# Performance work log

Hardware: AMD Instinct MI355X
Metric: run time of the kernel (lower is better)

The kernel has to match this reference:

```python
import jax, jax.numpy as jnp
import numpy as np

B, N, F_IN, D, NBLOCKS = 16, 1024, 3, 128, 15
EPS = 1e-5


def setup_inputs() -> dict:
    key = jax.random.key(0)
    ks = jax.random.split(key, 8)
    inputs = jax.random.normal(ks[0], (B, N, F_IN), dtype=jnp.float32)
    # Row-normalized random adjacency as the graph operator L (spectral norm <= 1)
    A = jax.random.uniform(ks[1], (B, N, N), dtype=jnp.float32)
    L = A / jnp.sum(A, axis=-1, keepdims=True)
    mask = (jax.random.uniform(ks[2], (B, N, 1)) < 0.8).astype(jnp.float32)
    mask = mask.at[:, 0, :].set(1.0)  # ensure no empty graph
    W1 = jax.random.normal(ks[3], (F_IN, D), dtype=jnp.float32) / np.sqrt(F_IN)
    b1 = jnp.zeros((D,), jnp.float32)
    W_blocks = jax.random.normal(ks[4], (NBLOCKS, D, D), dtype=jnp.float32) / np.sqrt(D)
    b_blocks = jnp.zeros((NBLOCKS, D), jnp.float32)
    gamma_blocks = jnp.ones((NBLOCKS, D), jnp.float32)
    beta_blocks = jnp.zeros((NBLOCKS, D), jnp.float32)
    gamma1 = jnp.ones((D,), jnp.float32)
    beta1 = jnp.zeros((D,), jnp.float32)
    gamma2 = jnp.ones((D,), jnp.float32)
    beta2 = jnp.zeros((D,), jnp.float32)
    W2 = jax.random.normal(ks[5], (D, D), dtype=jnp.float32) / np.sqrt(D)
    b2 = jnp.zeros((D,), jnp.float32)
    return dict(inputs=inputs, L=L, mask=mask, W1=W1, b1=b1,
                W_blocks=W_blocks, b_blocks=b_blocks,
                gamma_blocks=gamma_blocks, beta_blocks=beta_blocks,
                gamma1=gamma1, beta1=beta1, gamma2=gamma2, beta2=beta2,
                W2=W2, b2=b2)


def _graph_bn(x, gamma, beta):
    # BatchNorm over (batch, nodes) per feature channel (training-mode stats)
    mean = jnp.mean(x, axis=(0, 1), keepdims=True)
    var = jnp.var(x, axis=(0, 1), keepdims=True)
    return (x - mean) * jax.lax.rsqrt(var + EPS) * gamma + beta


def reference(inputs, L, mask, W1, b1, W_blocks, b_blocks,
              gamma_blocks, beta_blocks, gamma1, beta1, gamma2, beta2,
              W2, b2):
    # conv1 (GraphConv k=1): per-node linear
    x1 = jnp.einsum('bnf,fd->bnd', inputs, W1) + b1          # [B,N,D]
    x2 = jnp.zeros_like(x1)

    def step(carry, params):
        a, b_prev = carry
        W, bias, g, be = params
        h = jax.nn.elu(_graph_bn(a, g, be))
        h = jnp.einsum('bnm,bmd->bnd', L, h)                 # Laplacian aggregation
        h = jnp.einsum('bnd,de->bne', h, W) + bias           # LapConv transform
        return (b_prev + h, a), None

    (x1, x2), _ = jax.lax.scan(step, (x1, x2),
                               (W_blocks, b_blocks, gamma_blocks, beta_blocks))

    x = jax.nn.elu(_graph_bn(x1, gamma1, beta1) + _graph_bn(x2, gamma2, beta2))
    # Dropout2d is identity in deterministic/eval reference
    x = jnp.einsum('bnd,de->bne', x, W2) + b2                # conv2 (k=1)
    # masked mean pool over nodes: mask [B,N,1] broadcasts over D
    out = jnp.sum(x * mask, axis=1) / jnp.sum(mask, axis=1)  # [B,D]
    return out
```

## Files before the change

### kernel.cpp

```cpp
#include <hip/hip_runtime.h>

typedef float f32x4 __attribute__((ext_vector_type(4)));
typedef __bf16 bf16x8 __attribute__((ext_vector_type(8)));
typedef unsigned int u32x4 __attribute__((ext_vector_type(4)));
typedef unsigned int u32x2 __attribute__((ext_vector_type(2)));
typedef unsigned short u16;

#define DEV __device__ __forceinline__

DEV u16 f2bf(float f) {
    unsigned int x = __float_as_uint(f);
    x += 0x7fffu + ((x >> 16) & 1u);
    return (u16)(x >> 16);
}
DEV unsigned pk2(float a, float b) {
    return (unsigned)f2bf(a) | ((unsigned)f2bf(b) << 16);
}
DEV float elu(float x) { return x > 0.f ? x : expm1f(x); }

DEV void gload16(const u16* g, void* l) {
    __builtin_amdgcn_global_load_lds(
        (const __attribute__((address_space(1))) unsigned int*)g,
        (__attribute__((address_space(3))) unsigned int*)l,
        16, 0, 0);
}

constexpr float INV_M = 1.f / 16384.f;
constexpr float EPSV  = 1e-5f;


__global__ void k_cvt_bf16(const float* __restrict__ src, u16* __restrict__ dst) {
    long i = ((long)blockIdx.x * 256 + threadIdx.x) * 8;
    f32x4 a = *(const f32x4*)(src + i);
    f32x4 b = *(const f32x4*)(src + i + 4);
    u32x4 v;
    v[0] = pk2(a[0], a[1]); v[1] = pk2(a[2], a[3]);
    v[2] = pk2(b[0], b[1]); v[3] = pk2(b[2], b[3]);
    *(u32x4*)(dst + i) = v;
}

__global__ void k_cvt_wt(const float* __restrict__ W, u16* __restrict__ WT,
                         float* __restrict__ SP0, float* __restrict__ SP1) {
    int o = blockIdx.x * 256 + threadIdx.x;
    int k = o >> 14, r = o & 16383, e = r >> 7, d = r & 127;
    WT[o] = f2bf(W[(k << 14) + (d << 7) + e]);
    if (blockIdx.x < 32) {
        float* z = blockIdx.x < 16 ? SP0 : SP1;
        z[(blockIdx.x & 15) * 256 + threadIdx.x] = 0.f;
    }
}

__global__ __launch_bounds__(256) void k_init(
        const float* __restrict__ in, const float* __restrict__ W1,
        const float* __restrict__ b1, float* __restrict__ x1,
        float* __restrict__ x2, float* __restrict__ sp) {
    __shared__ float red[2][8][128];
    int t = threadIdx.x;
    long R = (long)blockIdx.x * 64;
    int c4 = (t & 31) * 4, rg = t >> 5;
    float w0[4], w1[4], w2[4], bb4[4];
#pragma unroll
    for (int c = 0; c < 4; ++c) {
        w0[c] = W1[c4 + c]; w1[c] = W1[128 + c4 + c]; w2[c] = W1[256 + c4 + c];
        bb4[c] = b1[c4 + c];
    }
    float s[4] = {}, q[4] = {};
    for (int i = 0; i < 8; ++i) {
        long grow = R + rg + 8 * i;
        float f0 = in[grow * 3], f1 = in[grow * 3 + 1], f2 = in[grow * 3 + 2];
        f32x4 v, z = {0.f, 0.f, 0.f, 0.f};
#pragma unroll
        for (int c = 0; c < 4; ++c) {
            float val = f0 * w0[c] + f1 * w1[c] + f2 * w2[c] + bb4[c];
            v[c] = val; s[c] += val; q[c] += val * val;
        }
        *(f32x4*)(x1 + grow * 128 + c4) = v;
        *(f32x4*)(x2 + grow * 128 + c4) = z;
    }
#pragma unroll
    for (int c = 0; c < 4; ++c) { red[0][rg][c4 + c] = s[c]; red[1][rg][c4 + c] = q[c]; }
    __syncthreads();
    if (t < 128) {
        float a = 0;
#pragma unroll
        for (int g = 0; g < 8; ++g) a += red[0][g][t];
        atomicAdd(&sp[(blockIdx.x & 15) * 256 + t], a);
    } else {
        int c = t - 128; float a = 0;
#pragma unroll
        for (int g = 0; g < 8; ++g) a += red[1][g][c];
        atomicAdd(&sp[(blockIdx.x & 15) * 256 + 128 + c], a);
    }
}


__global__ __launch_bounds__(256) void k_bnelu(
        const float* __restrict__ x, const float* __restrict__ spa,
        float* __restrict__ spb_zero,
        const float* __restrict__ gamma, const float* __restrict__ beta,
        const u16* __restrict__ WTk, u16* __restrict__ hT) {
    __shared__ u16 Hs[8192];
    __shared__ u16 Ws[16384];
    __shared__ float st[256];
    __shared__ float sc[128], sh[128];
    int t = threadIdx.x;
    int R = blockIdx.x * 64;  int bb = R >> 10, n0 = R & 1023;
    int l = t & 63, w = t >> 6;
    int wm = w >> 1, wn = w & 1;
    int l16 = l & 15, ld16 = l >> 4;

    {
        float s = 0.f;
#pragma unroll
        for (int i = 0; i < 16; ++i) s += spa[i * 256 + t];
        st[t] = s;
    }
    if (blockIdx.x < 16) spb_zero[blockIdx.x * 256 + t] = 0.f;

    {
        const u32x4* wsrc = (const u32x4*)WTk;
#pragma unroll
        for (int i = 0; i < 8; ++i) {
            int u = t + 256 * i;
            int r = u >> 4, sl = u & 15;
            *(u32x4*)((char*)Ws + r * 256 + ((sl ^ (r & 7)) << 4)) = wsrc[u];
        }
    }
    __syncthreads();
    if (t < 128) {
        float mean = st[t] * INV_M, var = st[128 + t] * INV_M - mean * mean;
        float a = rsqrtf(var + EPSV) * gamma[t];
        sc[t] = a; sh[t] = beta[t] - mean * a;
    }
    __syncthreads();

    {
        const float* xb = x + (long)R * 128;
#pragma unroll
        for (int i = 0; i < 8; ++i) {
            int idx = t + 256 * i;
            int row = idx >> 5, c4 = (idx & 31) * 4;
            f32x4 v = *(const f32x4*)(xb + row * 128 + c4);
            float h0 = elu(v[0] * sc[c4]     + sh[c4]);
            float h1 = elu(v[1] * sc[c4 + 1] + sh[c4 + 1]);
            float h2 = elu(v[2] * sc[c4 + 2] + sh[c4 + 2]);
            float h3 = elu(v[3] * sc[c4 + 3] + sh[c4 + 3]);
            u32x2 pw = {pk2(h0, h1), pk2(h2, h3)};
            *(u32x2*)((char*)Hs + row * 256 + ((c4 * 2) ^ ((row & 7) << 4))) = pw;
        }
    }
    __syncthreads();

    f32x4 acc[2][4] = {};
#pragma unroll
    for (int ks = 0; ks < 4; ++ks) {
        int kb = ks * 64 + ld16 * 16;
        bf16x8 af[2], bfr[4];
#pragma unroll
        for (int m = 0; m < 2; ++m) {
            int r = wm * 32 + m * 16 + l16;
            af[m] = *(const bf16x8*)((char*)Hs + r * 256 + (kb ^ ((r & 7) << 4)));
        }
#pragma unroll
        for (int n = 0; n < 4; ++n) {
            int e = wn * 64 + n * 16 + l16;
            bfr[n] = *(const bf16x8*)((char*)Ws + e * 256 + (kb ^ ((e & 7) << 4)));
        }
#pragma unroll
        for (int m = 0; m < 2; ++m)
#pragma unroll
            for (int n = 0; n < 4; ++n)
                acc[m][n] = __builtin_amdgcn_mfma_f32_16x16x32_bf16(
                    af[m], bfr[n], acc[m][n], 0, 0, 0);
    }
    __syncthreads();

#pragma unroll
    for (int m = 0; m < 2; ++m)
#pragma unroll
        for (int n = 0; n < 4; ++n) {
            int e = wn * 64 + n * 16 + l16;
            int row0 = wm * 32 + m * 16 + ld16 * 4;
            u32x2 pw = {pk2(acc[m][n][0], acc[m][n][1]),
                        pk2(acc[m][n][2], acc[m][n][3])};
            *(u32x2*)((char*)Hs + e * 128 + ((row0 * 2) ^ ((e & 7) << 4))) = pw;
        }
    __syncthreads();

    {
        int e = t >> 1, sg = t & 1;
        const char* base = (const char*)Hs + e * 128;
        u16* orow = hT + ((long)(bb * 128 + e)) * 1024 + n0 + sg * 32;
#pragma unroll
        for (int u = 0; u < 4; ++u) {
            u32x4 v = *(const u32x4*)(base + ((((sg * 4 + u) * 16)) ^ ((e & 7) << 4)));
            *(u32x4*)(orow + u * 8) = v;
        }
    }
}

__global__ __launch_bounds__(512) void k_gemm(
        const u16* __restrict__ Lb, const u16* __restrict__ hT,
        const float* __restrict__ bias, float* __restrict__ xio,
        float* __restrict__ spb) {
    __shared__ u16 As[3][4096];
    __shared__ u16 Bs[3][8192];
    __shared__ float red[2][8][128];

    int t = threadIdx.x;
    int bid0 = blockIdx.x;
    int wg = ((bid0 & 7) << 5) | (bid0 >> 3);
    int bb = wg >> 4, n0 = (wg & 15) << 6;
    int l = t & 63, w = t >> 6;
    int wm = w >> 2, wn = w & 3;
    int l16 = l & 15, ld16 = l >> 4;

    const u16* gA = Lb + ((long)(bb * 1024 + n0)) * 1024;
    const u16* gB = hT + (long)bb * 131072;

#define STAGE(buf, kt) do {                                                   \
        int k0_ = (kt) * 64;                                                  \
        { int u = t; int r = u >> 3, sl = u & 7;                              \
          gload16(gA + (long)r * 1024 + k0_ + ((sl ^ (r & 7)) << 3),          \
                  (char*)As[buf] + u * 16); }                                 \
        _Pragma("unroll")                                                     \
        for (int j = 0; j < 2; ++j) {                                         \
            int u = t + 512 * j; int r = u >> 3, sl = u & 7;                  \
            gload16(gB + (long)r * 1024 + k0_ + ((sl ^ (r & 7)) << 3),        \
                    (char*)Bs[buf] + u * 16);                                 \
        }                                                                     \
    } while (0)

    f32x4 acc[2][2] = {};

    STAGE(0, 0);
    STAGE(1, 1);
    asm volatile("s_waitcnt vmcnt(3)" ::: "memory");
    __builtin_amdgcn_s_barrier();

    for (int kt = 0; kt < 16; ++kt) {
        if (kt <= 13) STAGE((kt + 2) % 3, kt + 2);
        const char* Ab = (const char*)(As[kt % 3]);
        const char* Bb = (const char*)(Bs[kt % 3]);
        __builtin_amdgcn_s_setprio(1);
#pragma unroll
        for (int ks = 0; ks < 2; ++ks) {
            int kb = ks * 64 + ld16 * 16;
            bf16x8 af[2], bfr[2];
#pragma unroll
            for (int m = 0; m < 2; ++m) {
                int r = wm * 32 + m * 16 + l16;
                af[m] = *(const bf16x8*)(Ab + r * 128 + (kb ^ ((r & 7) << 4)));
            }
#pragma unroll
            for (int n = 0; n < 2; ++n) {
                int e = wn * 32 + n * 16 + l16;
                bfr[n] = *(const bf16x8*)(Bb + e * 128 + (kb ^ ((e & 7) << 4)));
            }
#pragma unroll
            for (int m = 0; m < 2; ++m)
#pragma unroll
                for (int n = 0; n < 2; ++n)
                    acc[m][n] = __builtin_amdgcn_mfma_f32_16x16x32_bf16(
                        af[m], bfr[n], acc[m][n], 0, 0, 0);
        }
        __builtin_amdgcn_s_setprio(0);
        if (kt <= 13) {
            asm volatile("s_waitcnt vmcnt(3)" ::: "memory");
            __builtin_amdgcn_s_barrier();
        } else if (kt == 14) {
            asm volatile("s_waitcnt vmcnt(0)" ::: "memory");
            __builtin_amdgcn_s_barrier();
        }
    }
#undef STAGE

    float* dst = xio + (long)(bb * 1024 + n0) * 128;
#pragma unroll
    for (int n = 0; n < 2; ++n) {
        int e = wn * 32 + n * 16 + l16;
        float bv = bias[e];
        float sv = 0.f, qv = 0.f;
#pragma unroll
        for (int m = 0; m < 2; ++m) {
            int row0 = wm * 32 + m * 16 + ld16 * 4;
            float* dp = dst + (long)row0 * 128 + e;
#pragma unroll
            for (int j = 0; j < 4; ++j) {
                float v = dp[j * 128] + acc[m][n][j] + bv;
                dp[j * 128] = v;
                sv += v; qv += v * v;
            }
        }
        red[0][wm * 4 + ld16][e] = sv;
        red[1][wm * 4 + ld16][e] = qv;
    }
    __syncthreads();
    if (t < 128) {
        float a = 0;
#pragma unroll
        for (int g = 0; g < 8; ++g) a += red[0][g][t];
        atomicAdd(&spb[(bid0 & 15) * 256 + t], a);
    } else if (t < 256) {
        int c = t - 128; float a = 0;
#pragma unroll
        for (int g = 0; g < 8; ++g) a += red[1][g][c];
        atomicAdd(&spb[(bid0 & 15) * 256 + 128 + c], a);
    }
}


__global__ void k_redstats2(const float* __restrict__ sp1, const float* __restrict__ sp0,
                            const float* __restrict__ g1, const float* __restrict__ be1,
                            const float* __restrict__ g2, const float* __restrict__ be2,
                            float* __restrict__ scb2) {
    int t = threadIdx.x;
    int which = t >> 7, c = t & 127;
    const float* p = which ? sp0 : sp1;
    float s = 0.f, q = 0.f;
#pragma unroll
    for (int i = 0; i < 16; ++i) { s += p[i * 256 + c]; q += p[i * 256 + 128 + c]; }
    float mean = s * INV_M, var = q * INV_M - mean * mean;
    const float* g = which ? g2 : g1; const float* be = which ? be2 : be1;
    float a = rsqrtf(var + EPSV) * g[c];
    scb2[which * 256 + c] = a;
    scb2[which * 256 + 128 + c] = be[c] - mean * a;
}

__global__ void k_finalpool(const float* __restrict__ x1, const float* __restrict__ x2,
                            const float* __restrict__ scb2, const float* __restrict__ mask,
                            float* __restrict__ poolP, float* __restrict__ maskP) {
    __shared__ float sc1[128], sh1[128], sc2[128], sh2[128];
    __shared__ float red[8][128];
    __shared__ float msk[64];
    int t = threadIdx.x;
    int R = blockIdx.x * 64, bb = R >> 10, tl = (R & 1023) >> 6;
    if (t < 128) {
        sc1[t] = scb2[t];       sh1[t] = scb2[128 + t];
        sc2[t] = scb2[256 + t]; sh2[t] = scb2[384 + t];
    }
    if (t >= 128 && t < 192) msk[t - 128] = mask[bb * 1024 + (R & 1023) + (t - 128)];
    __syncthreads();
    const float* xb1 = x1 + (long)R * 128;
    const float* xb2 = x2 + (long)R * 128;
    int row0 = t >> 5, c = (t & 31) * 4;
    f32x4 accv = {0.f, 0.f, 0.f, 0.f};
    for (int i = 0; i < 8; ++i) {
        int row = row0 + 8 * i;
        f32x4 v1 = *(const f32x4*)(xb1 + row * 128 + c);
        f32x4 v2 = *(const f32x4*)(xb2 + row * 128 + c);
        float m = msk[row];
        accv[0] += elu(v1[0]*sc1[c]   + sh1[c]   + v2[0]*sc2[c]   + sh2[c])   * m;
        accv[1] += elu(v1[1]*sc1[c+1] + sh1[c+1] + v2[1]*sc2[c+1] + sh2[c+1]) * m;
        accv[2] += elu(v1[2]*sc1[c+2] + sh1[c+2] + v2[2]*sc2[c+2] + sh2[c+2]) * m;
        accv[3] += elu(v1[3]*sc1[c+3] + sh1[c+3] + v2[3]*sc2[c+3] + sh2[c+3]) * m;
    }
    red[row0][c] = accv[0]; red[row0][c+1] = accv[1];
    red[row0][c+2] = accv[2]; red[row0][c+3] = accv[3];
    __syncthreads();
    if (t < 128) {
        float s = 0;
#pragma unroll
        for (int g = 0; g < 8; ++g) s += red[g][t];
        poolP[(bb * 16 + tl) * 128 + t] = s;
    }
    if (t == 0) {
        float sm = 0;
        for (int j = 0; j < 64; ++j) sm += msk[j];
        maskP[bb * 16 + tl] = sm;
    }
}

__global__ void k_out(const float* __restrict__ poolP, const float* __restrict__ maskP,
                      const float* __restrict__ W2, const float* __restrict__ b2,
                      float* __restrict__ out) {
    int bb = blockIdx.x, t = threadIdx.x;
    __shared__ float pooled[128];
    __shared__ float inv;
    float s = 0;
    for (int tl = 0; tl < 16; ++tl) s += poolP[(bb * 16 + tl) * 128 + t];
    pooled[t] = s;
    if (t == 0) {
        float sm = 0;
        for (int tl = 0; tl < 16; ++tl) sm += maskP[bb * 16 + tl];
        inv = 1.f / sm;
    }
    __syncthreads();
    float acc = 0;
    for (int d = 0; d < 128; ++d) acc += pooled[d] * W2[d * 128 + t];
    out[bb * 128 + t] = acc * inv + b2[t];
}


extern "C" void kernel_launch(void* const* d_in, const int* in_sizes, int n_in,
                              void* d_out, int out_size, void* d_ws, size_t ws_size,
                              hipStream_t stream) {
    const float* inputs = (const float*)d_in[0];
    const float* L      = (const float*)d_in[1];
    const float* mask   = (const float*)d_in[2];
    const float* W1     = (const float*)d_in[3];
    const float* b1     = (const float*)d_in[4];
    const float* Wb     = (const float*)d_in[5];
    const float* bblk   = (const float*)d_in[6];
    const float* gb     = (const float*)d_in[7];
    const float* beb    = (const float*)d_in[8];
    const float* g1     = (const float*)d_in[9];
    const float* be1    = (const float*)d_in[10];
    const float* g2     = (const float*)d_in[11];
    const float* be2    = (const float*)d_in[12];
    const float* W2     = (const float*)d_in[13];
    const float* b2     = (const float*)d_in[14];
    float* out = (float*)d_out;

    char* ws = (char*)d_ws;
    u16*   Lb    = (u16*)(ws);
    u16*   WT    = (u16*)(ws + 33554432);
    float* xA    = (float*)(ws + 34045952);
    float* xB    = (float*)(ws + 42434560);
    u16*   hT    = (u16*)(ws + 50823168);
    float* SP0   = (float*)(ws + 55017472);
    float* SP1   = (float*)(ws + 55279616);
    float* scb2  = (float*)(ws + 55542784);
    float* poolP = (float*)(ws + 50823168);
    float* maskP = (float*)(ws + 50823168 + 131072);
    float* SP[2] = {SP0, SP1};

    hipLaunchKernelGGL(k_cvt_bf16, dim3(8192), dim3(256), 0, stream, L, Lb);
    hipLaunchKernelGGL(k_cvt_wt,   dim3(960),  dim3(256), 0, stream, Wb, WT, SP0, SP1);
    hipLaunchKernelGGL(k_init,     dim3(256),  dim3(256), 0, stream,
                       inputs, W1, b1, xA, xB, SP0);

    float* pa = xA; float* pb = xB;
    for (int k = 0; k < 15; ++k) {
        hipLaunchKernelGGL(k_bnelu, dim3(256), dim3(256), 0, stream,
                           pa, SP[k & 1], SP[(k + 1) & 1],
                           gb + k * 128, beb + k * 128,
                           WT + (size_t)k * 16384, hT);
        hipLaunchKernelGGL(k_gemm, dim3(256), dim3(512), 0, stream,
                           Lb, hT, bblk + k * 128, pb, SP[(k + 1) & 1]);
        float* tmp = pa; pa = pb; pb = tmp;
    }
    hipLaunchKernelGGL(k_redstats2, dim3(1), dim3(256), 0, stream,
                       SP[1], SP[0], g1, be1, g2, be2, scb2);
    hipLaunchKernelGGL(k_finalpool, dim3(256), dim3(256), 0, stream,
                       pa, pb, scb2, mask, poolP, maskP);
    hipLaunchKernelGGL(k_out, dim3(16), dim3(128), 0, stream, poolP, maskP, W2, b2, out);
}
```

Before: 394.0 us.

## Fuse all stages into one persistent kernel with software grid barriers

Replaces the sequence of about 35 kernel launches (conversion, init, 15 pairs of bnelu and gemm, final stats, pool, output) with one persistent 256-block kernel that separates phases with an atomic-counter grid barrier. The goal is to remove launch overhead and the inter-kernel gaps between the many short stages. The bnelu stage now runs with 512 threads per block and a different warp tiling, and the final stats are computed redundantly per block. In exchange it relies on all 256 blocks being co-resident, and adds spin-wait barrier cost at every phase.

```diff
diff --git a/kernel.cpp b/kernel.cpp
--- a/kernel.cpp
+++ b/kernel.cpp
@@ -25,370 +25,372 @@
         16, 0, 0);
 }
 
+DEV void gridbar(unsigned* bar) {
+    __syncthreads();
+    if (threadIdx.x == 0) {
+        __builtin_amdgcn_fence(__ATOMIC_RELEASE, "agent");
+        unsigned old = __hip_atomic_fetch_add(bar, 1u, __ATOMIC_RELAXED,
+                                              __HIP_MEMORY_SCOPE_AGENT);
+        unsigned target = ((old >> 8) << 8) + 256u;
+        while (__hip_atomic_load(bar, __ATOMIC_RELAXED,
+                                 __HIP_MEMORY_SCOPE_AGENT) < target)
+            __builtin_amdgcn_s_sleep(2);
+        __builtin_amdgcn_fence(__ATOMIC_ACQUIRE, "agent");
+    }
+    __syncthreads();
+}
+
 constexpr float INV_M = 1.f / 16384.f;
 constexpr float EPSV  = 1e-5f;
 
-
-__global__ void k_cvt_bf16(const float* __restrict__ src, u16* __restrict__ dst) {
-    long i = ((long)blockIdx.x * 256 + threadIdx.x) * 8;
-    f32x4 a = *(const f32x4*)(src + i);
-    f32x4 b = *(const f32x4*)(src + i + 4);
-    u32x4 v;
-    v[0] = pk2(a[0], a[1]); v[1] = pk2(a[2], a[3]);
-    v[2] = pk2(b[0], b[1]); v[3] = pk2(b[2], b[3]);
-    *(u32x4*)(dst + i) = v;
-}
-
-__global__ void k_cvt_wt(const float* __restrict__ W, u16* __restrict__ WT,
-                         float* __restrict__ SP0, float* __restrict__ SP1) {
-    int o = blockIdx.x * 256 + threadIdx.x;
-    int k = o >> 14, r = o & 16383, e = r >> 7, d = r & 127;
-    WT[o] = f2bf(W[(k << 14) + (d << 7) + e]);
-    if (blockIdx.x < 32) {
-        float* z = blockIdx.x < 16 ? SP0 : SP1;
-        z[(blockIdx.x & 15) * 256 + threadIdx.x] = 0.f;
-    }
-}
-
-__global__ __launch_bounds__(256) void k_init(
-        const float* __restrict__ in, const float* __restrict__ W1,
-        const float* __restrict__ b1, float* __restrict__ x1,
-        float* __restrict__ x2, float* __restrict__ sp) {
-    __shared__ float red[2][8][128];
+__global__ __launch_bounds__(512) void k_mega(
+        const float* __restrict__ in, const float* __restrict__ L,
+        const float* __restrict__ mask, const float* __restrict__ W1,
+        const float* __restrict__ b1, const float* __restrict__ Wb,
+        const float* __restrict__ bblk, const float* __restrict__ gb,
+        const float* __restrict__ beb, const float* __restrict__ g1,
+        const float* __restrict__ be1, const float* __restrict__ g2,
+        const float* __restrict__ be2, const float* __restrict__ W2,
+        const float* __restrict__ b2,
+        u16* __restrict__ Lb, u16* __restrict__ WT,
+        float* __restrict__ xA, float* __restrict__ xB,
+        u16* __restrict__ hT, float* __restrict__ SP0, float* __restrict__ SP1,
+        unsigned* __restrict__ bar, float* __restrict__ poolP,
+        float* __restrict__ maskP, float* __restrict__ out) {
+    extern __shared__ char smem[];
     int t = threadIdx.x;
-    long R = (long)blockIdx.x * 64;
-    int c4 = (t & 31) * 4, rg = t >> 5;
-    float w0[4], w1[4], w2[4], bb4[4];
-#pragma unroll
-    for (int c = 0; c < 4; ++c) {
-        w0[c] = W1[c4 + c]; w1[c] = W1[128 + c4 + c]; w2[c] = W1[256 + c4 + c];
-        bb4[c] = b1[c4 + c];
-    }
-    float s[4] = {}, q[4] = {};
-    for (int i = 0; i < 8; ++i) {
-        long grow = R + rg + 8 * i;
-        float f0 = in[grow * 3], f1 = in[grow * 3 + 1], f2 = in[grow * 3 + 2];
-        f32x4 v, z = {0.f, 0.f, 0.f, 0.f};
-#pragma unroll
-        for (int c = 0; c < 4; ++c) {
-            float val = f0 * w0[c] + f1 * w1[c] + f2 * w2[c] + bb4[c];
-            v[c] = val; s[c] += val; q[c] += val * val;
-        }
-        *(f32x4*)(x1 + grow * 128 + c4) = v;
-        *(f32x4*)(x2 + grow * 128 + c4) = z;
-    }
-#pragma unroll
-    for (int c = 0; c < 4; ++c) { red[0][rg][c4 + c] = s[c]; red[1][rg][c4 + c] = q[c]; }
-    __syncthreads();
-    if (t < 128) {
-        float a = 0;
-#pragma unroll
-        for (int g = 0; g < 8; ++g) a += red[0][g][t];
-        atomicAdd(&sp[(blockIdx.x & 15) * 256 + t], a);
-    } else {
-        int c = t - 128; float a = 0;
-#pragma unroll
-        for (int g = 0; g < 8; ++g) a += red[1][g][c];
-        atomicAdd(&sp[(blockIdx.x & 15) * 256 + 128 + c], a);
-    }
-}
-
-
-__global__ __launch_bounds__(256) void k_bnelu(
-        const float* __restrict__ x, const float* __restrict__ spa,
-        float* __restrict__ spb_zero,
-        const float* __restrict__ gamma, const float* __restrict__ beta,
-        const u16* __restrict__ WTk, u16* __restrict__ hT) {
-    __shared__ u16 Hs[8192];
-    __shared__ u16 Ws[16384];
-    __shared__ float st[256];
-    __shared__ float sc[128], sh[128];
-    int t = threadIdx.x;
-    int R = blockIdx.x * 64;  int bb = R >> 10, n0 = R & 1023;
-    int l = t & 63, w = t >> 6;
-    int wm = w >> 1, wn = w & 1;
-    int l16 = l & 15, ld16 = l >> 4;
-
-    {
-        float s = 0.f;
-#pragma unroll
-        for (int i = 0; i < 16; ++i) s += spa[i * 256 + t];
-        st[t] = s;
-    }
-    if (blockIdx.x < 16) spb_zero[blockIdx.x * 256 + t] = 0.f;
-
-    {
-        const u32x4* wsrc = (const u32x4*)WTk;
-#pragma unroll
-        for (int i = 0; i < 8; ++i) {
-            int u = t + 256 * i;
-            int r = u >> 4, sl = u & 15;
-            *(u32x4*)((char*)Ws + r * 256 + ((sl ^ (r & 7)) << 4)) = wsrc[u];
-        }
-    }
-    __syncthreads();
-    if (t < 128) {
-        float mean = st[t] * INV_M, var = st[128 + t] * INV_M - mean * mean;
-        float a = rsqrtf(var + EPSV) * gamma[t];
-        sc[t] = a; sh[t] = beta[t] - mean * a;
-    }
-    __syncthreads();
-
-    {
-        const float* xb = x + (long)R * 128;
-#pragma unroll
-        for (int i = 0; i < 8; ++i) {
-            int idx = t + 256 * i;
-            int row = idx >> 5, c4 = (idx & 31) * 4;
-            f32x4 v = *(const f32x4*)(xb + row * 128 + c4);
-            float h0 = elu(v[0] * sc[c4]     + sh[c4]);
-            float h1 = elu(v[1] * sc[c4 + 1] + sh[c4 + 1]);
-            float h2 = elu(v[2] * sc[c4 + 2] + sh[c4 + 2]);
-            float h3 = elu(v[3] * sc[c4 + 3] + sh[c4 + 3]);
-            u32x2 pw = {pk2(h0, h1), pk2(h2, h3)};
-            *(u32x2*)((char*)Hs + row * 256 + ((c4 * 2) ^ ((row & 7) << 4))) = pw;
-        }
-    }
-    __syncthreads();
-
-    f32x4 acc[2][4] = {};
-#pragma unroll
-    for (int ks = 0; ks < 4; ++ks) {
-        int kb = ks * 64 + ld16 * 16;
-        bf16x8 af[2], bfr[4];
-#pragma unroll
-        for (int m = 0; m < 2; ++m) {
-            int r = wm * 32 + m * 16 + l16;
-            af[m] = *(const bf16x8*)((char*)Hs + r * 256 + (kb ^ ((r & 7) << 4)));
-        }
-#pragma unroll
-        for (int n = 0; n < 4; ++n) {
-            int e = wn * 64 + n * 16 + l16;
-            bfr[n] = *(const bf16x8*)((char*)Ws + e * 256 + (kb ^ ((e & 7) << 4)));
-        }
-#pragma unroll
-        for (int m = 0; m < 2; ++m)
-#pragma unroll
-            for (int n = 0; n < 4; ++n)
-                acc[m][n] = __builtin_amdgcn_mfma_f32_16x16x32_bf16(
-                    af[m], bfr[n], acc[m][n], 0, 0, 0);
-    }
-    __syncthreads();
-
-#pragma unroll
-    for (int m = 0; m < 2; ++m)
-#pragma unroll
-        for (int n = 0; n < 4; ++n) {
-            int e = wn * 64 + n * 16 + l16;
-            int row0 = wm * 32 + m * 16 + ld16 * 4;
-            u32x2 pw = {pk2(acc[m][n][0], acc[m][n][1]),
-                        pk2(acc[m][n][2], acc[m][n][3])};
-            *(u32x2*)((char*)Hs + e * 128 + ((row0 * 2) ^ ((e & 7) << 4))) = pw;
-        }
-    __syncthreads();
-
-    {
-        int e = t >> 1, sg = t & 1;
-        const char* base = (const char*)Hs + e * 128;
-        u16* orow = hT + ((long)(bb * 128 + e)) * 1024 + n0 + sg * 32;
-#pragma unroll
-        for (int u = 0; u < 4; ++u) {
-            u32x4 v = *(const u32x4*)(base + ((((sg * 4 + u) * 16)) ^ ((e & 7) << 4)));
-            *(u32x4*)(orow + u * 8) = v;
-        }
-    }
-}
-
-__global__ __launch_bounds__(512) void k_gemm(
-        const u16* __restrict__ Lb, const u16* __restrict__ hT,
-        const float* __restrict__ bias, float* __restrict__ xio,
-        float* __restrict__ spb) {
-    __shared__ u16 As[3][4096];
-    __shared__ u16 Bs[3][8192];
-    __shared__ float red[2][8][128];
-
-    int t = threadIdx.x;
-    int bid0 = blockIdx.x;
-    int wg = ((bid0 & 7) << 5) | (bid0 >> 3);
+    int bid = blockIdx.x;
+    int wg = ((bid & 7) << 5) | (bid >> 3);
     int bb = wg >> 4, n0 = (wg & 15) << 6;
     int l = t & 63, w = t >> 6;
     int wm = w >> 2, wn = w & 3;
     int l16 = l & 15, ld16 = l >> 4;
 
-    const u16* gA = Lb + ((long)(bb * 1024 + n0)) * 1024;
-    const u16* gB = hT + (long)bb * 131072;
-
-#define STAGE(buf, kt) do {                                                   \
-        int k0_ = (kt) * 64;                                                  \
-        { int u = t; int r = u >> 3, sl = u & 7;                              \
-          gload16(gA + (long)r * 1024 + k0_ + ((sl ^ (r & 7)) << 3),          \
-                  (char*)As[buf] + u * 16); }                                 \
-        _Pragma("unroll")                                                     \
-        for (int j = 0; j < 2; ++j) {                                         \
-            int u = t + 512 * j; int r = u >> 3, sl = u & 7;                  \
-            gload16(gB + (long)r * 1024 + k0_ + ((sl ^ (r & 7)) << 3),        \
-                    (char*)Bs[buf] + u * 16);                                 \
-        }                                                                     \
-    } while (0)
-
-    f32x4 acc[2][2] = {};
-
-    STAGE(0, 0);
-    STAGE(1, 1);
-    asm volatile("s_waitcnt vmcnt(3)" ::: "memory");
-    __builtin_amdgcn_s_barrier();
-
-    for (int kt = 0; kt < 16; ++kt) {
-        if (kt <= 13) STAGE((kt + 2) % 3, kt + 2);
-        const char* Ab = (const char*)(As[kt % 3]);
-        const char* Bb = (const char*)(Bs[kt % 3]);
-        __builtin_amdgcn_s_setprio(1);
-#pragma unroll
-        for (int ks = 0; ks < 2; ++ks) {
-            int kb = ks * 64 + ld16 * 16;
-            bf16x8 af[2], bfr[2];
-#pragma unroll
-            for (int m = 0; m < 2; ++m) {
-                int r = wm * 32 + m * 16 + l16;
-                af[m] = *(const bf16x8*)(Ab + r * 128 + (kb ^ ((r & 7) << 4)));
-            }
+    {
+        for (long v = (long)bid * 512 + t; v < 2097152; v += 131072) {
+            long i = v * 8;
+            f32x4 a = *(const f32x4*)(L + i);
+            f32x4 b = *(const f32x4*)(L + i + 4);
+            u32x4 pv;
+            pv[0] = pk2(a[0], a[1]); pv[1] = pk2(a[2], a[3]);
+            pv[2] = pk2(b[0], b[1]); pv[3] = pk2(b[2], b[3]);
+            *(u32x4*)(Lb + i) = pv;
+        }
+        for (int o = bid * 512 + t; o < 245760; o += 131072) {
+            int k = o >> 14, r = o & 16383, e = r >> 7, d = r & 127;
+            WT[o] = f2bf(Wb[(k << 14) + (d << 7) + e]);
+        }
+        float* red0 = (float*)smem;
+        float* red1 = (float*)(smem + 8192);
+        int c4 = (t & 31) * 4, rg = t >> 5;
+        float w0[4], w1v[4], w2v[4], bb4[4];
+#pragma unroll
+        for (int c = 0; c < 4; ++c) {
+            w0[c] = W1[c4 + c]; w1v[c] = W1[128 + c4 + c];
+            w2v[c] = W1[256 + c4 + c]; bb4[c] = b1[c4 + c];
+        }
+        float s[4] = {}, q[4] = {};
+        long R = (long)wg * 64;
+#pragma unroll
+        for (int i = 0; i < 4; ++i) {
+            long grow = R + rg + 16 * i;
+            float f0 = in[grow * 3], f1 = in[grow * 3 + 1], f2 = in[grow * 3 + 2];
+            f32x4 v, z = {0.f, 0.f, 0.f, 0.f};
+#pragma unroll
+            for (int c = 0; c < 4; ++c) {
+                float val = f0 * w0[c] + f1 * w1v[c] + f2 * w2v[c] + bb4[c];
+                v[c] = val; s[c] += val; q[c] += val * val;
+            }
+            *(f32x4*)(xA + grow * 128 + c4) = v;
+            *(f32x4*)(xB + grow * 128 + c4) = z;
+        }
+#pragma unroll
+        for (int c = 0; c < 4; ++c) {
+            red0[rg * 128 + c4 + c] = s[c]; red1[rg * 128 + c4 + c] = q[c];
+        }
+        __syncthreads();
+        if (t < 128) {
+            float a = 0;
+#pragma unroll
+            for (int g = 0; g < 16; ++g) a += red0[g * 128 + t];
+            atomicAdd(&SP0[(wg & 15) * 256 + t], a);
+        } else if (t < 256) {
+            int c = t - 128; float a = 0;
+#pragma unroll
+            for (int g = 0; g < 16; ++g) a += red1[g * 128 + c];
+            atomicAdd(&SP0[(wg & 15) * 256 + 128 + c], a);
+        }
+    }
+    gridbar(bar);
+
+    float* pa = xA; float* pb = xB;
+    for (int k = 0; k < 15; ++k) {
+        float* spa = (k & 1) ? SP1 : SP0;
+        float* spb = (k & 1) ? SP0 : SP1;
+
+        {
+            u16* Ws = (u16*)smem;
+            u16* Hs = (u16*)(smem + 32768);
+            float* st = (float*)(smem + 49152);
+            float* sc = (float*)(smem + 50176);
+            float* sh = (float*)(smem + 50688);
+            if (t < 256) {
+                float s = 0.f;
+#pragma unroll
+                for (int i = 0; i < 16; ++i) s += spa[i * 256 + t];
+                st[t] = s;
+            }
+            if (wg < 16 && t < 256) spb[wg * 256 + t] = 0.f;
+            const u32x4* wsrc = (const u32x4*)(WT + (size_t)k * 16384);
+#pragma unroll
+            for (int i = 0; i < 4; ++i) {
+                int u = t + 512 * i;
+                int r = u >> 4, sl = u & 15;
+                *(u32x4*)((char*)Ws + r * 256 + ((sl ^ (r & 7)) << 4)) = wsrc[u];
+            }
+            __syncthreads();
+            if (t < 128) {
+                float mean = st[t] * INV_M, var = st[128 + t] * INV_M - mean * mean;
+                float a = rsqrtf(var + EPSV) * gb[k * 128 + t];
+                sc[t] = a; sh[t] = beb[k * 128 + t] - mean * a;
+            }
+            __syncthreads();
+            const float* xb = pa + (long)wg * 8192;
+#pragma unroll
+            for (int i = 0; i < 4; ++i) {
+                int idx = t + 512 * i;
+                int row = idx >> 5, c4 = (idx & 31) * 4;
+                f32x4 v = *(const f32x4*)(xb + row * 128 + c4);
+                float h0 = elu(v[0] * sc[c4]     + sh[c4]);
+                float h1 = elu(v[1] * sc[c4 + 1] + sh[c4 + 1]);
+                float h2 = elu(v[2] * sc[c4 + 2] + sh[c4 + 2]);
+                float h3 = elu(v[3] * sc[c4 + 3] + sh[c4 + 3]);
+                u32x2 pw = {pk2(h0, h1), pk2(h2, h3)};
+                *(u32x2*)((char*)Hs + row * 256 + ((c4 * 2) ^ ((row & 7) << 4))) = pw;
+            }
+            __syncthreads();
+            f32x4 acc[2][2] = {};
+#pragma unroll
+            for (int ks = 0; ks < 4; ++ks) {
+                int kb = ks * 64 + ld16 * 16;
+                bf16x8 af[2], bfr[2];
+#pragma unroll
+                for (int m = 0; m < 2; ++m) {
+                    int r = wm * 32 + m * 16 + l16;
+                    af[m] = *(const bf16x8*)((char*)Hs + r * 256 + (kb ^ ((r & 7) << 4)));
+                }
+#pragma unroll
+                for (int n = 0; n < 2; ++n) {
+                    int e = wn * 32 + n * 16 + l16;
+                    bfr[n] = *(const bf16x8*)((char*)Ws + e * 256 + (kb ^ ((e & 7) << 4)));
+                }
+#pragma unroll
+                for (int m = 0; m < 2; ++m)
+#pragma unroll
+                    for (int n = 0; n < 2; ++n)
+                        acc[m][n] = __builtin_amdgcn_mfma_f32_16x16x32_bf16(
+                            af[m], bfr[n], acc[m][n], 0, 0, 0);
+            }
+            __syncthreads();
+#pragma unroll
+            for (int m = 0; m < 2; ++m)
+#pragma unroll
+                for (int n = 0; n < 2; ++n) {
+                    int e = wn * 32 + n * 16 + l16;
+                    int row0 = wm * 32 + m * 16 + ld16 * 4;
+                    u32x2 pw = {pk2(acc[m][n][0], acc[m][n][1]),
+                                pk2(acc[m][n][2], acc[m][n][3])};
+                    *(u32x2*)((char*)Hs + e * 128 + ((row0 * 2) ^ ((e & 7) << 4))) = pw;
+                }
+            __syncthreads();
+            {
+                int e = t >> 2, sg = t & 3;
+                const char* base = (const char*)Hs + e * 128;
+                u16* orow = hT + ((long)(bb * 128 + e)) * 1024 + n0 + sg * 16;
+#pragma unroll
+                for (int u = 0; u < 2; ++u) {
+                    u32x4 v = *(const u32x4*)(base + ((sg * 32 + u * 16) ^ ((e & 7) << 4)));
+                    *(u32x4*)(orow + u * 8) = v;
+                }
+            }
+        }
+        gridbar(bar);
+
+        {
+            u16* As = (u16*)smem;
+            u16* Bs = (u16*)(smem + 24576);
+            float* red = (float*)(smem + 40960);
+            const u16* gA = Lb + ((long)(bb * 1024 + n0)) * 1024;
+            const u16* gB = hT + (long)bb * 131072;
+
+#define STAGE(buf, kt_) do {                                                  \
+            int k0_ = (kt_) * 64;                                             \
+            { int u = t; int r = u >> 3, sl = u & 7;                          \
+              gload16(gA + (long)r * 1024 + k0_ + ((sl ^ (r & 7)) << 3),      \
+                      (char*)As + (buf) * 8192 + u * 16); }                   \
+            _Pragma("unroll")                                                 \
+            for (int j = 0; j < 2; ++j) {                                     \
+                int u = t + 512 * j; int r = u >> 3, sl = u & 7;              \
+                gload16(gB + (long)r * 1024 + k0_ + ((sl ^ (r & 7)) << 3),    \
+                        (char*)Bs + (buf) * 16384 + u * 16);                  \
+            }                                                                 \
+        } while (0)
+
+            f32x4 acc[2][2] = {};
+            STAGE(0, 0);
+            STAGE(1, 1);
+            asm volatile("s_waitcnt vmcnt(3)" ::: "memory");
+            __builtin_amdgcn_s_barrier();
+
+            for (int kt = 0; kt < 16; ++kt) {
+                if (kt <= 13) STAGE((kt + 2) % 3, kt + 2);
+                const char* Ab = (const char*)As + (kt % 3) * 8192;
+                const char* Bb = (const char*)Bs + (kt % 3) * 16384;
+                __builtin_amdgcn_s_setprio(1);
+#pragma unroll
+                for (int ks = 0; ks < 2; ++ks) {
+                    int kb = ks * 64 + ld16 * 16;
+                    bf16x8 af[2], bfr[2];
+#pragma unroll
+                    for (int m = 0; m < 2; ++m) {
+                        int r = wm * 32 + m * 16 + l16;
+                        af[m] = *(const bf16x8*)(Ab + r * 128 + (kb ^ ((r & 7) << 4)));
+                    }
+#pragma unroll
+                    for (int n = 0; n < 2; ++n) {
+                        int e = wn * 32 + n * 16 + l16;
+                        bfr[n] = *(const bf16x8*)(Bb + e * 128 + (kb ^ ((e & 7) << 4)));
+                    }
+#pragma unroll
+                    for (int m = 0; m < 2; ++m)
+#pragma unroll
+                        for (int n = 0; n < 2; ++n)
+                            acc[m][n] = __builtin_amdgcn_mfma_f32_16x16x32_bf16(
+                                af[m], bfr[n], acc[m][n], 0, 0, 0);
+                }
+                __builtin_amdgcn_s_setprio(0);
+                if (kt <= 13) {
+                    asm volatile("s_waitcnt vmcnt(3)" ::: "memory");
+                    __builtin_amdgcn_s_barrier();
+                } else if (kt == 14) {
+                    asm volatile("s_waitcnt vmcnt(0)" ::: "memory");
+                    __builtin_amdgcn_s_barrier();
+                }
+            }
+#undef STAGE
+
+            float* dst = pb + (long)wg * 8192;
 #pragma unroll
             for (int n = 0; n < 2; ++n) {
                 int e = wn * 32 + n * 16 + l16;
-                bfr[n] = *(const bf16x8*)(Bb + e * 128 + (kb ^ ((e & 7) << 4)));
-            }
-#pragma unroll
-            for (int m = 0; m < 2; ++m)
-#pragma unroll
-                for (int n = 0; n < 2; ++n)
-                    acc[m][n] = __builtin_amdgcn_mfma_f32_16x16x32_bf16(
-                        af[m], bfr[n], acc[m][n], 0, 0, 0);
-        }
-        __builtin_amdgcn_s_setprio(0);
-        if (kt <= 13) {
-            asm volatile("s_waitcnt vmcnt(3)" ::: "memory");
-            __builtin_amdgcn_s_barrier();
-        } else if (kt == 14) {
-            asm volatile("s_waitcnt vmcnt(0)" ::: "memory");
-            __builtin_amdgcn_s_barrier();
-        }
+                float bv = bblk[k * 128 + e];
+                float sv = 0.f, qv = 0.f;
+#pragma unroll
+                for (int m = 0; m < 2; ++m) {
+                    int row0 = wm * 32 + m * 16 + ld16 * 4;
+                    float* dp = dst + (long)row0 * 128 + e;
+#pragma unroll
+                    for (int j = 0; j < 4; ++j) {
+                        float v = dp[j * 128] + acc[m][n][j] + bv;
+                        dp[j * 128] = v;
+                        sv += v; qv += v * v;
+                    }
+                }
+                red[(wm * 4 + ld16) * 128 + e] = sv;
+                red[(8 + wm * 4 + ld16) * 128 + e] = qv;
+            }
+            __syncthreads();
+            if (t < 128) {
+                float a = 0;
+#pragma unroll
+                for (int g = 0; g < 8; ++g) a += red[g * 128 + t];
+                atomicAdd(&spb[(wg & 15) * 256 + t], a);
+            } else if (t < 256) {
+                int c = t - 128; float a = 0;
+#pragma unroll
+                for (int g = 0; g < 8; ++g) a += red[(8 + g) * 128 + c];
+                atomicAdd(&spb[(wg & 15) * 256 + 128 + c], a);
+            }
+        }
+        gridbar(bar);
+        float* tmp = pa; pa = pb; pb = tmp;
     }
-#undef STAGE
-
-    float* dst = xio + (long)(bb * 1024 + n0) * 128;
-#pragma unroll
-    for (int n = 0; n < 2; ++n) {
-        int e = wn * 32 + n * 16 + l16;
-        float bv = bias[e];
-        float sv = 0.f, qv = 0.f;
-#pragma unroll
-        for (int m = 0; m < 2; ++m) {
-            int row0 = wm * 32 + m * 16 + ld16 * 4;
-            float* dp = dst + (long)row0 * 128 + e;
-#pragma unroll
-            for (int j = 0; j < 4; ++j) {
-                float v = dp[j * 128] + acc[m][n][j] + bv;
-                dp[j * 128] = v;
-                sv += v; qv += v * v;
-            }
-        }
-        red[0][wm * 4 + ld16][e] = sv;
-        red[1][wm * 4 + ld16][e] = qv;
+
+    {
+        float* sc1 = (float*)smem;
+        float* sh1 = sc1 + 128;
+        float* sc2 = sh1 + 128;
+        float* sh2 = sc2 + 128;
+        float* msk = (float*)(smem + 2048);
+        float* fred = (float*)(smem + 4096);
+        if (t < 256) {
+            int which = t >> 7, c = t & 127;
+            const float* p = which ? SP0 : SP1;
+            float s = 0.f, q = 0.f;
+#pragma unroll
+            for (int i = 0; i < 16; ++i) { s += p[i * 256 + c]; q += p[i * 256 + 128 + c]; }
+            float mean = s * INV_M, var = q * INV_M - mean * mean;
+            float a = rsqrtf(var + EPSV) * (which ? g2[c] : g1[c]);
+            (which ? sc2 : sc1)[c] = a;
+            (which ? sh2 : sh1)[c] = (which ? be2[c] : be1[c]) - mean * a;
+        } else if (t < 320) {
+            msk[t - 256] = mask[bb * 1024 + n0 + (t - 256)];
+        }
+        __syncthreads();
+        const float* xb1 = pa + (long)wg * 8192;
+        const float* xb2 = pb + (long)wg * 8192;
+        int row0 = t >> 5, c = (t & 31) * 4;
+        f32x4 accv = {0.f, 0.f, 0.f, 0.f};
+#pragma unroll
+        for (int i = 0; i < 4; ++i) {
+            int row = row0 + 16 * i;
+            f32x4 v1 = *(const f32x4*)(xb1 + row * 128 + c);
+            f32x4 v2 = *(const f32x4*)(xb2 + row * 128 + c);
+            float m = msk[row];
+            accv[0] += elu(v1[0]*sc1[c]   + sh1[c]   + v2[0]*sc2[c]   + sh2[c])   * m;
+            accv[1] += elu(v1[1]*sc1[c+1] + sh1[c+1] + v2[1]*sc2[c+1] + sh2[c+1]) * m;
+            accv[2] += elu(v1[2]*sc1[c+2] + sh1[c+2] + v2[2]*sc2[c+2] + sh2[c+2]) * m;
+            accv[3] += elu(v1[3]*sc1[c+3] + sh1[c+3] + v2[3]*sc2[c+3] + sh2[c+3]) * m;
+        }
+        fred[row0 * 128 + c]     = accv[0];
+        fred[row0 * 128 + c + 1] = accv[1];
+        fred[row0 * 128 + c + 2] = accv[2];
+        fred[row0 * 128 + c + 3] = accv[3];
+        __syncthreads();
+        if (t < 128) {
+            float s = 0;
+#pragma unroll
+            for (int g = 0; g < 16; ++g) s += fred[g * 128 + t];
+            poolP[wg * 128 + t] = s;
+        }
+        if (t == 128) {
+            float sm = 0;
+#pragma unroll
+            for (int j = 0; j < 64; ++j) sm += msk[j];
+            maskP[wg] = sm;
+        }
     }
-    __syncthreads();
-    if (t < 128) {
-        float a = 0;
-#pragma unroll
-        for (int g = 0; g < 8; ++g) a += red[0][g][t];
-        atomicAdd(&spb[(bid0 & 15) * 256 + t], a);
-    } else if (t < 256) {
-        int c = t - 128; float a = 0;
-#pragma unroll
-        for (int g = 0; g < 8; ++g) a += red[1][g][c];
-        atomicAdd(&spb[(bid0 & 15) * 256 + 128 + c], a);
+    gridbar(bar);
+
+    if (wg < 16) {
+        float* pooled = (float*)smem;
+        if (t < 128) {
+            float s = 0.f;
+            for (int tl = 0; tl < 16; ++tl) s += poolP[(wg * 16 + tl) * 128 + t];
+            pooled[t] = s;
+        }
+        if (t == 128) {
+            float sm = 0.f;
+            for (int tl = 0; tl < 16; ++tl) sm += maskP[wg * 16 + tl];
+            pooled[128] = 1.f / sm;
+        }
+        __syncthreads();
+        if (t < 128) {
+            float acc = 0.f, inv = pooled[128];
+            for (int d = 0; d < 128; ++d) acc += pooled[d] * W2[d * 128 + t];
+            out[wg * 128 + t] = acc * inv + b2[t];
+        }
     }
-}
-
-
-__global__ void k_redstats2(const float* __restrict__ sp1, const float* __restrict__ sp0,
-                            const float* __restrict__ g1, const float* __restrict__ be1,
-                            const float* __restrict__ g2, const float* __restrict__ be2,
-                            float* __restrict__ scb2) {
-    int t = threadIdx.x;
-    int which = t >> 7, c = t & 127;
-    const float* p = which ? sp0 : sp1;
-    float s = 0.f, q = 0.f;
-#pragma unroll
-    for (int i = 0; i < 16; ++i) { s += p[i * 256 + c]; q += p[i * 256 + 128 + c]; }
-    float mean = s * INV_M, var = q * INV_M - mean * mean;
-    const float* g = which ? g2 : g1; const float* be = which ? be2 : be1;
-    float a = rsqrtf(var + EPSV) * g[c];
-    scb2[which * 256 + c] = a;
-    scb2[which * 256 + 128 + c] = be[c] - mean * a;
-}
-
-__global__ void k_finalpool(const float* __restrict__ x1, const float* __restrict__ x2,
-                            const float* __restrict__ scb2, const float* __restrict__ mask,
-                            float* __restrict__ poolP, float* __restrict__ maskP) {
-    __shared__ float sc1[128], sh1[128], sc2[128], sh2[128];
-    __shared__ float red[8][128];
-    __shared__ float msk[64];
-    int t = threadIdx.x;
-    int R = blockIdx.x * 64, bb = R >> 10, tl = (R & 1023) >> 6;
-    if (t < 128) {
-        sc1[t] = scb2[t];       sh1[t] = scb2[128 + t];
-        sc2[t] = scb2[256 + t]; sh2[t] = scb2[384 + t];
-    }
-    if (t >= 128 && t < 192) msk[t - 128] = mask[bb * 1024 + (R & 1023) + (t - 128)];
-    __syncthreads();
-    const float* xb1 = x1 + (long)R * 128;
-    const float* xb2 = x2 + (long)R * 128;
-    int row0 = t >> 5, c = (t & 31) * 4;
-    f32x4 accv = {0.f, 0.f, 0.f, 0.f};
-    for (int i = 0; i < 8; ++i) {
-        int row = row0 + 8 * i;
-        f32x4 v1 = *(const f32x4*)(xb1 + row * 128 + c);
-        f32x4 v2 = *(const f32x4*)(xb2 + row * 128 + c);
-        float m = msk[row];
-        accv[0] += elu(v1[0]*sc1[c]   + sh1[c]   + v2[0]*sc2[c]   + sh2[c])   * m;
-        accv[1] += elu(v1[1]*sc1[c+1] + sh1[c+1] + v2[1]*sc2[c+1] + sh2[c+1]) * m;
-        accv[2] += elu(v1[2]*sc1[c+2] + sh1[c+2] + v2[2]*sc2[c+2] + sh2[c+2]) * m;
-        accv[3] += elu(v1[3]*sc1[c+3] + sh1[c+3] + v2[3]*sc2[c+3] + sh2[c+3]) * m;
-    }
-    red[row0][c] = accv[0]; red[row0][c+1] = accv[1];
-    red[row0][c+2] = accv[2]; red[row0][c+3] = accv[3];
-    __syncthreads();
-    if (t < 128) {
-        float s = 0;
-#pragma unroll
-        for (int g = 0; g < 8; ++g) s += red[g][t];
-        poolP[(bb * 16 + tl) * 128 + t] = s;
-    }
-    if (t == 0) {
-        float sm = 0;
-        for (int j = 0; j < 64; ++j) sm += msk[j];
-        maskP[bb * 16 + tl] = sm;
-    }
-}
-
-__global__ void k_out(const float* __restrict__ poolP, const float* __restrict__ maskP,
-                      const float* __restrict__ W2, const float* __restrict__ b2,
-                      float* __restrict__ out) {
-    int bb = blockIdx.x, t = threadIdx.x;
-    __shared__ float pooled[128];
-    __shared__ float inv;
-    float s = 0;
-    for (int tl = 0; tl < 16; ++tl) s += poolP[(bb * 16 + tl) * 128 + t];
-    pooled[t] = s;
-    if (t == 0) {
-        float sm = 0;
-        for (int tl = 0; tl < 16; ++tl) sm += maskP[bb * 16 + tl];
-        inv = 1.f / sm;
-    }
-    __syncthreads();
-    float acc = 0;
-    for (int d = 0; d < 128; ++d) acc += pooled[d] * W2[d * 128 + t];
-    out[bb * 128 + t] = acc * inv + b2[t];
 }
 
 
@@ -413,36 +415,21 @@
     float* out = (float*)d_out;
 
     char* ws = (char*)d_ws;
-    u16*   Lb    = (u16*)(ws);
-    u16*   WT    = (u16*)(ws + 33554432);
-    float* xA    = (float*)(ws + 34045952);
-    float* xB    = (float*)(ws + 42434560);
-    u16*   hT    = (u16*)(ws + 50823168);
-    float* SP0   = (float*)(ws + 55017472);
-    float* SP1   = (float*)(ws + 55279616);
-    float* scb2  = (float*)(ws + 55542784);
-    float* poolP = (float*)(ws + 50823168);
-    float* maskP = (float*)(ws + 50823168 + 131072);
-    float* SP[2] = {SP0, SP1};
-
-    hipLaunchKernelGGL(k_cvt_bf16, dim3(8192), dim3(256), 0, stream, L, Lb);
-    hipLaunchKernelGGL(k_cvt_wt,   dim3(960),  dim3(256), 0, stream, Wb, WT, SP0, SP1);
-    hipLaunchKernelGGL(k_init,     dim3(256),  dim3(256), 0, stream,
-                       inputs, W1, b1, xA, xB, SP0);
-
-    float* pa = xA; float* pb = xB;
-    for (int k = 0; k < 15; ++k) {
-        hipLaunchKernelGGL(k_bnelu, dim3(256), dim3(256), 0, stream,
-                           pa, SP[k & 1], SP[(k + 1) & 1],
-                           gb + k * 128, beb + k * 128,
-                           WT + (size_t)k * 16384, hT);
-        hipLaunchKernelGGL(k_gemm, dim3(256), dim3(512), 0, stream,
-                           Lb, hT, bblk + k * 128, pb, SP[(k + 1) & 1]);
-        float* tmp = pa; pa = pb; pb = tmp;
-    }
-    hipLaunchKernelGGL(k_redstats2, dim3(1), dim3(256), 0, stream,
-                       SP[1], SP[0], g1, be1, g2, be2, scb2);
-    hipLaunchKernelGGL(k_finalpool, dim3(256), dim3(256), 0, stream,
-                       pa, pb, scb2, mask, poolP, maskP);
-    hipLaunchKernelGGL(k_out, dim3(16), dim3(128), 0, stream, poolP, maskP, W2, b2, out);
-}
+    u16*      Lb    = (u16*)(ws);
+    u16*      WT    = (u16*)(ws + 33554432);
+    float*    xA    = (float*)(ws + 34045952);
+    float*    xB    = (float*)(ws + 42434560);
+    u16*      hT    = (u16*)(ws + 50823168);
+    float*    poolP = (float*)(ws + 50823168);
+    float*    maskP = (float*)(ws + 50823168 + 131072);
+    float*    SP0   = (float*)(ws + 55017472);
+    float*    SP1   = (float*)(ws + 55017472 + 16384);
+    unsigned* bar   = (unsigned*)(ws + 55017472 + 32768);
+
+    hipMemsetAsync(ws + 55017472, 0, 32768 + 256, stream);
+
+    hipLaunchKernelGGL(k_mega, dim3(256), dim3(512), 73728, stream,
+                       inputs, L, mask, W1, b1, Wb, bblk, gb, beb,
+                       g1, be1, g2, be2, W2, b2,
+                       Lb, WT, xA, xB, hT, SP0, SP1, bar, poolP, maskP, out);
+}
```

Result: slower. 765.6 us (+94.3%).
